# Kernel tuning notes

Hardware: AMD Instinct MI355X
Metric: run time of the kernel (lower is better)

The kernel has to match this reference:

```python
import jax, jax.numpy as jnp
import numpy as np

POOLED_H = 7
POOLED_W = 7
SPATIAL_SCALE = 0.0625
B, C, H, W = 8, 256, 48, 48
R = 300
IMG = 768  # = H / SPATIAL_SCALE


def setup_inputs() -> dict:
    key = jax.random.key(0)
    k1, k2, k3, k4 = jax.random.split(key, 4)
    features = jax.random.normal(k1, (B, C, H, W), dtype=jnp.float32)
    # rois: (batch_idx, x1, y1, x2, y2) in input-image coords
    bidx = jax.random.randint(k2, (R, 1), 0, B).astype(jnp.float32)
    tl = jax.random.uniform(k3, (R, 2), minval=0.0, maxval=IMG - 64.0)
    wh = jax.random.uniform(k4, (R, 2), minval=32.0, maxval=320.0)
    br = jnp.minimum(tl + wh, IMG - 1.0)
    rois = jnp.concatenate([bidx, tl, br], axis=1).astype(jnp.float32)
    return {"features": features, "rois": rois}


def _hat_integral(x, grid):
    """Integral from -inf to x of the unit hat basis function centered at each
    grid point g (support [g-1, g+1], peak 1, total mass 1).
    x: [..., 1-broadcastable], grid: [G] -> returns [..., G]."""
    t = x[..., None] - (grid - 1.0)
    return jnp.where(
        t <= 0.0, 0.0,
        jnp.where(t <= 1.0, 0.5 * t * t,
                  jnp.where(t <= 2.0, 1.0 - 0.5 * (2.0 - t) ** 2, 1.0)))


def reference(features, rois):
    # Precise RoI Pooling: exact double integral of the bilinear interpolant
    # over each bin, divided by bin area. Bilinear interp (with zero padding
    # outside the map, as in the CUDA PrRoIPoolingGetData) is
    #   f(u,v) = sum_{j,i} feat[j,i] * hat_j(v) * hat_i(u)
    # so the bin integral factorizes into per-axis hat-integral weights.
    Bf, Cf, Hf, Wf = features.shape
    bidx = rois[:, 0].astype(jnp.int32)
    x1 = rois[:, 1] * SPATIAL_SCALE
    y1 = rois[:, 2] * SPATIAL_SCALE
    x2 = rois[:, 3] * SPATIAL_SCALE
    y2 = rois[:, 4] * SPATIAL_SCALE
    roi_w = jnp.maximum(x2 - x1, 0.0)
    roi_h = jnp.maximum(y2 - y1, 0.0)
    bin_w = roi_w / POOLED_W  # [R]
    bin_h = roi_h / POOLED_H

    ph = jnp.arange(POOLED_H, dtype=jnp.float32)
    pw = jnp.arange(POOLED_W, dtype=jnp.float32)
    ya = y1[:, None] + ph[None, :] * bin_h[:, None]  # [R, PH]
    yb = ya + bin_h[:, None]
    xa = x1[:, None] + pw[None, :] * bin_w[:, None]  # [R, PW]
    xb = xa + bin_w[:, None]

    gy = jnp.arange(Hf, dtype=jnp.float32)
    gx = jnp.arange(Wf, dtype=jnp.float32)
    Wy = _hat_integral(yb, gy) - _hat_integral(ya, gy)  # [R, PH, H]
    Wx = _hat_integral(xb, gx) - _hat_integral(xa, gx)  # [R, PW, W]

    feat = features[bidx]  # [R, C, H, W]
    t = jnp.einsum('rpj,rcji->rcpi', Wy, feat)   # integrate over y
    num = jnp.einsum('rqi,rcpi->rcpq', Wx, t)    # integrate over x -> [R,C,PH,PW]

    area = (bin_w * bin_h)[:, None, None, None]  # win_size per ROI
    out = jnp.where(area > 0.0, num / jnp.where(area > 0.0, area, 1.0), 0.0)
    return out
```

## Files before the change

kernel.cpp:

```cpp
#include <hip/hip_runtime.h>


#define PH 7
#define PW 7
#define NBINS 49
#define SCALE 0.0625f
#define CH 256
#define FH 48
#define FW 48
#define RNUM 300
#define MAXJ 23
#define PRM 112
#define PATCHF (MAXJ * 28 * 2)
#define RSF 328

__device__ __forceinline__ float hat_int(float x, float g) {
    float t = x - (g - 1.0f);
    if (t <= 0.0f) return 0.0f;
    if (t <= 1.0f) return 0.5f * t * t;
    if (t <= 2.0f) { float u = 2.0f - t; return 1.0f - 0.5f * u * u; }
    return 1.0f;
}

__global__ __launch_bounds__(256)
void prroi_prep(const float* __restrict__ rois, float* __restrict__ prm) {
    const int r = blockIdx.x * 4 + (threadIdx.x >> 6);
    const int t = threadIdx.x & 63;
    if (r >= RNUM || t >= 15) return;

    const float* roi = rois + r * 5;
    const int   b  = (int)roi[0];
    const float x1 = roi[1] * SCALE, y1 = roi[2] * SCALE;
    const float x2 = roi[3] * SCALE, y2 = roi[4] * SCALE;
    const float roi_w = fmaxf(x2 - x1, 0.0f), roi_h = fmaxf(y2 - y1, 0.0f);
    const float bin_w = roi_w / (float)PW, bin_h = roi_h / (float)PH;
    const float area = bin_w * bin_h;
    const float inv_area = (area > 0.0f) ? (1.0f / area) : 0.0f;

    const float ylo = fminf(y1, y2), yhi = fmaxf(y1, y2);
    const float xlo = fminf(x1, x2), xhi = fmaxf(x1, x2);
    const int j1 = min(FH - 1, (int)floorf(yhi) + 1);
    const int i1 = min(FW - 1, (int)floorf(xhi) + 1);
    const int J0 = min(max(0, (int)floorf(ylo) - 1), FH - 6);
    const int I0 = min(max(0, (int)floorf(xlo) - 1) & ~3, FW - 8);
    const int JROWS = min(FH - J0, max(j1 - J0 + 1, 6));
    int NI4 = min(((i1 - I0) >> 2) + 1, (FW - I0) >> 2);
    NI4 = max(NI4, 2);

    float* p = prm + (size_t)r * PRM;
    if (t < PH) {
        const int ph = t;
        const float ya = y1 + ph * bin_h, yb = ya + bin_h;
        const int base = min(max((int)floorf(ya) - 1, J0), J0 + JROWS - 6);
        p[84 + ph] = __int_as_float(base - J0);
#pragma unroll
        for (int k = 0; k < 6; ++k) {
            const float g = (float)(base + k);
            p[ph * 6 + k] = hat_int(yb, g) - hat_int(ya, g);
        }
    } else if (t < PH + PW) {
        const int pw = t - PH;
        const float xa = x1 + pw * bin_w, xb = xa + bin_w;
        const int base = min(max((int)floorf(xa) - 1, I0), I0 + 4 * NI4 - 6);
        p[91 + pw] = __int_as_float(base - I0);
#pragma unroll
        for (int k = 0; k < 6; ++k) {
            const float g = (float)(base + k);
            p[42 + pw * 6 + k] = hat_int(xb, g) - hat_int(xa, g);
        }
    } else {
        p[98]  = inv_area;
        p[99]  = __int_as_float(b);
        p[100] = __int_as_float(J0);
        p[101] = __int_as_float(I0);
        p[102] = __int_as_float(JROWS);
        p[103] = __int_as_float(NI4);
    }
}

__global__ __launch_bounds__(256, 6)
void prroi_main(const float* __restrict__ feat,
                const float* __restrict__ prm,
                float* __restrict__ out) {
    const int wv   = threadIdx.x >> 6;
    const int lane = threadIdx.x & 63;
    const int r    = blockIdx.y;
    const int cblk = blockIdx.x * 4 + wv;
    const int c0   = cblk * 2;

    __shared__ float lds[4][PATCHF + RSF];
    float* patch = lds[wv];
    float* rsw   = lds[wv] + PATCHF;

    const float* p = prm + (size_t)r * PRM;
    const int b     = __float_as_int(p[99]);
    const int J0    = __float_as_int(p[100]);
    const int I0    = __float_as_int(p[101]);
    const int JROWS = __float_as_int(p[102]);
    const int NI4   = __float_as_int(p[103]);
    const float ia  = p[98];

    const int pwA = lane >> 3;
    const int jsl = lane & 7;
    const bool actA = lane < 56;
    float wx[6]; int bi = 0;
    if (actA) {
        bi = __float_as_int(p[91 + pwA]);
#pragma unroll
        for (int k = 0; k < 6; ++k) wx[k] = p[42 + pwA * 6 + k];
    }
    const bool actB = lane < NBINS;
    int bj = 0, pwB = 0;
    float wy[6];
    if (actB) {
        const int ph = lane / 7;
        pwB = lane - ph * 7;
        bj = __float_as_int(p[84 + ph]);
#pragma unroll
        for (int k = 0; k < 6; ++k) wy[k] = p[ph * 6 + k];
    }

    const float* fb = feat + (size_t)(b * CH + c0) * (FH * FW);
    const int NU = JROWS << 3;
    for (int u = lane; u < NU; u += 64) {
        const int j = u >> 3, i4 = u & 7;
        if (i4 < NI4) {
            const float* src = fb + (size_t)(J0 + j) * FW + I0 + 4 * i4;
            const float4 a = *(const float4*)src;
            const float4 c = *(const float4*)(src + FH * FW);
            const int base = j * 56 + 8 * i4;
            const int sw = (j & 7) << 1;
            *(float2*)&patch[(base + 0) ^ sw] = make_float2(a.x, c.x);
            *(float2*)&patch[(base + 2) ^ sw] = make_float2(a.y, c.y);
            *(float2*)&patch[(base + 4) ^ sw] = make_float2(a.z, c.z);
            *(float2*)&patch[(base + 6) ^ sw] = make_float2(a.w, c.w);
        }
    }
    asm volatile("s_waitcnt lgkmcnt(0)" ::: "memory");

    if (actA) {
        for (int j = jsl; j < JROWS; j += 8) {
            const int rowb = j * 56 + 2 * bi;
            const int sw = (j & 7) << 1;
            float ax = 0.0f, ay = 0.0f;
#pragma unroll
            for (int ii = 0; ii < 6; ++ii) {
                const float2 v = *(const float2*)&patch[(rowb + 2 * ii) ^ sw];
                ax += wx[ii] * v.x; ay += wx[ii] * v.y;
            }
            *(float2*)&rsw[(pwA * MAXJ + j) * 2] = make_float2(ax, ay);
        }
    }
    asm volatile("s_waitcnt lgkmcnt(0)" ::: "memory");

    if (actB) {
        float ax = 0.0f, ay = 0.0f;
#pragma unroll
        for (int jj = 0; jj < 6; ++jj) {
            const float2 v = *(const float2*)&rsw[(pwB * MAXJ + (bj + jj)) * 2];
            ax += wy[jj] * v.x; ay += wy[jj] * v.y;
        }
        float* o = out + ((size_t)r * CH + c0) * NBINS + lane;
        o[0]     = ax * ia;
        o[NBINS] = ay * ia;
    }
}

extern "C" void kernel_launch(void* const* d_in, const int* in_sizes, int n_in,
                              void* d_out, int out_size, void* d_ws, size_t ws_size,
                              hipStream_t stream) {
    const float* feat = (const float*)d_in[0];
    const float* rois = (const float*)d_in[1];
    float* out = (float*)d_out;
    float* prm = (float*)d_ws;

    prroi_prep<<<(RNUM + 3) / 4, 256, 0, stream>>>(rois, prm);
    prroi_main<<<dim3(32, RNUM), 256, 0, stream>>>(feat, prm, out);
}
```

Measured before the change: 86.36 us.

## Group ROIs by batch and reuse full feature map in LDS across ROIs

The prep kernel gains an extra block that builds per-batch ROI lists and counts. The main kernel now launches one block per (batch, channel pair), loads the whole 48x48 map for two channels into LDS once, and loops over every ROI of that batch. Before, each ROI block fetched its own patch, so the same feature data was read repeatedly from global memory. In exchange, ROI counts per batch are uneven, which causes load imbalance, and the grid shrinks to 1024 blocks of 128 threads, each using a large LDS allocation that limits occupancy.

```diff
diff --git a/kernel.cpp b/kernel.cpp
--- a/kernel.cpp
+++ b/kernel.cpp
@@ -9,10 +9,10 @@
 #define FH 48
 #define FW 48
 #define RNUM 300
-#define MAXJ 23
 #define PRM 112
-#define PATCHF (MAXJ * 28 * 2)
-#define RSF 328
+#define PRMF (RNUM * PRM)
+#define LISTCAP 304
+#define RSF 332
 
 __device__ __forceinline__ float hat_int(float x, float g) {
     float t = x - (g - 1.0f);
@@ -24,6 +24,27 @@
 
 __global__ __launch_bounds__(256)
 void prroi_prep(const float* __restrict__ rois, float* __restrict__ prm) {
+    if (blockIdx.x == 75) {
+        __shared__ int lb[RNUM];
+        int* lst = (int*)(prm + PRMF);
+        int* cnt = lst + 8 * LISTCAP;
+        const int tid = threadIdx.x;
+        for (int u = tid; u < RNUM; u += 256) lb[u] = (int)rois[5 * u];
+        __syncthreads();
+        for (int u = tid; u < RNUM; u += 256) {
+            const int bu = lb[u];
+            int pos = 0;
+            for (int r2 = 0; r2 < u; ++r2) pos += (lb[r2] == bu) ? 1 : 0;
+            lst[bu * LISTCAP + pos] = u;
+        }
+        if (tid < 8) {
+            int c = 0;
+            for (int r2 = 0; r2 < RNUM; ++r2) c += (lb[r2] == tid) ? 1 : 0;
+            cnt[tid] = c;
+        }
+        return;
+    }
+
     const int r = blockIdx.x * 4 + (threadIdx.x >> 6);
     const int t = threadIdx.x & 63;
     if (r >= RNUM || t >= 15) return;
@@ -78,91 +99,93 @@
     }
 }
 
-__global__ __launch_bounds__(256, 6)
+__global__ __launch_bounds__(128, 2)
 void prroi_main(const float* __restrict__ feat,
                 const float* __restrict__ prm,
                 float* __restrict__ out) {
-    const int wv   = threadIdx.x >> 6;
-    const int lane = threadIdx.x & 63;
-    const int r    = blockIdx.y;
-    const int cblk = blockIdx.x * 4 + wv;
-    const int c0   = cblk * 2;
-
-    __shared__ float lds[4][PATCHF + RSF];
-    float* patch = lds[wv];
-    float* rsw   = lds[wv] + PATCHF;
-
-    const float* p = prm + (size_t)r * PRM;
-    const int b     = __float_as_int(p[99]);
-    const int J0    = __float_as_int(p[100]);
-    const int I0    = __float_as_int(p[101]);
-    const int JROWS = __float_as_int(p[102]);
-    const int NI4   = __float_as_int(p[103]);
-    const float ia  = p[98];
-
-    const int pwA = lane >> 3;
-    const int jsl = lane & 7;
+    const int bid = blockIdx.x;
+    const int b   = bid >> 7;
+    const int c2  = bid & 127;
+    const int c0  = c2 * 2;
+    const int tid = threadIdx.x;
+    const int wv  = tid >> 6, lane = tid & 63;
+
+    __shared__ float patch[FH * FW * 2];
+    __shared__ float rsw[2][RSF];
+
+    const float* fb = feat + (size_t)(b * CH + c0) * (FH * FW);
+    for (int u = tid; u < (FH * FW / 4); u += 128) {
+        const int j  = u / 12;
+        const float4 a = *(const float4*)(fb + u * 4);
+        const float4 c = *(const float4*)(fb + FH * FW + u * 4);
+        const int o0 = u * 8;
+        const int sw = (j & 7) << 2;
+        *(float2*)&patch[(o0 + 0) ^ sw] = make_float2(a.x, c.x);
+        *(float2*)&patch[(o0 + 2) ^ sw] = make_float2(a.y, c.y);
+        *(float2*)&patch[(o0 + 4) ^ sw] = make_float2(a.z, c.z);
+        *(float2*)&patch[(o0 + 6) ^ sw] = make_float2(a.w, c.w);
+    }
+    __syncthreads();
+
+    const int* lst = (const int*)(prm + PRMF);
+    const int cnt  = lst[8 * LISTCAP + b];
+    float* rsme = rsw[wv];
+
+    const int  pwA  = lane >> 3, jsl = lane & 7;
     const bool actA = lane < 56;
-    float wx[6]; int bi = 0;
-    if (actA) {
-        bi = __float_as_int(p[91 + pwA]);
-#pragma unroll
-        for (int k = 0; k < 6; ++k) wx[k] = p[42 + pwA * 6 + k];
-    }
     const bool actB = lane < NBINS;
-    int bj = 0, pwB = 0;
-    float wy[6];
-    if (actB) {
-        const int ph = lane / 7;
-        pwB = lane - ph * 7;
-        bj = __float_as_int(p[84 + ph]);
-#pragma unroll
-        for (int k = 0; k < 6; ++k) wy[k] = p[ph * 6 + k];
-    }
-
-    const float* fb = feat + (size_t)(b * CH + c0) * (FH * FW);
-    const int NU = JROWS << 3;
-    for (int u = lane; u < NU; u += 64) {
-        const int j = u >> 3, i4 = u & 7;
-        if (i4 < NI4) {
-            const float* src = fb + (size_t)(J0 + j) * FW + I0 + 4 * i4;
-            const float4 a = *(const float4*)src;
-            const float4 c = *(const float4*)(src + FH * FW);
-            const int base = j * 56 + 8 * i4;
-            const int sw = (j & 7) << 1;
-            *(float2*)&patch[(base + 0) ^ sw] = make_float2(a.x, c.x);
-            *(float2*)&patch[(base + 2) ^ sw] = make_float2(a.y, c.y);
-            *(float2*)&patch[(base + 4) ^ sw] = make_float2(a.z, c.z);
-            *(float2*)&patch[(base + 6) ^ sw] = make_float2(a.w, c.w);
-        }
-    }
-    asm volatile("s_waitcnt lgkmcnt(0)" ::: "memory");
-
-    if (actA) {
-        for (int j = jsl; j < JROWS; j += 8) {
-            const int rowb = j * 56 + 2 * bi;
-            const int sw = (j & 7) << 1;
+    int phB = 0, pwB = 0;
+    if (actB) { phB = lane / 7; pwB = lane - phB * 7; }
+
+    for (int k = wv; k < cnt; k += 2) {
+        const int r = lst[b * LISTCAP + k];
+        const float* p = prm + (size_t)r * PRM;
+        const float ia = p[98];
+        const int J0    = __float_as_int(p[100]);
+        const int I0    = __float_as_int(p[101]);
+        const int JROWS = __float_as_int(p[102]);
+
+        float wx[6]; int biA = 0;
+        if (actA) {
+            biA = I0 + __float_as_int(p[91 + pwA]);
+#pragma unroll
+            for (int t6 = 0; t6 < 6; ++t6) wx[t6] = p[42 + pwA * 6 + t6];
+        }
+        float wy[6]; int bj = 0;
+        if (actB) {
+            bj = __float_as_int(p[84 + phB]);
+#pragma unroll
+            for (int t6 = 0; t6 < 6; ++t6) wy[t6] = p[phB * 6 + t6];
+        }
+
+        if (actA) {
+            for (int jr = jsl; jr < JROWS; jr += 8) {
+                const int j  = J0 + jr;
+                const int o0 = (j * FW + biA) * 2;
+                const int sw = (j & 7) << 2;
+                float ax = 0.0f, ay = 0.0f;
+#pragma unroll
+                for (int ii = 0; ii < 6; ++ii) {
+                    const float2 v = *(const float2*)&patch[(o0 + 2 * ii) ^ sw];
+                    ax += wx[ii] * v.x; ay += wx[ii] * v.y;
+                }
+                *(float2*)&rsme[(pwA * 23 + jr) * 2] = make_float2(ax, ay);
+            }
+        }
+        asm volatile("s_waitcnt lgkmcnt(0)" ::: "memory");
+
+        if (actB) {
             float ax = 0.0f, ay = 0.0f;
 #pragma unroll
-            for (int ii = 0; ii < 6; ++ii) {
-                const float2 v = *(const float2*)&patch[(rowb + 2 * ii) ^ sw];
-                ax += wx[ii] * v.x; ay += wx[ii] * v.y;
+            for (int jj = 0; jj < 6; ++jj) {
+                const float2 v = *(const float2*)&rsme[(pwB * 23 + bj + jj) * 2];
+                ax += wy[jj] * v.x; ay += wy[jj] * v.y;
             }
-            *(float2*)&rsw[(pwA * MAXJ + j) * 2] = make_float2(ax, ay);
-        }
-    }
-    asm volatile("s_waitcnt lgkmcnt(0)" ::: "memory");
-
-    if (actB) {
-        float ax = 0.0f, ay = 0.0f;
-#pragma unroll
-        for (int jj = 0; jj < 6; ++jj) {
-            const float2 v = *(const float2*)&rsw[(pwB * MAXJ + (bj + jj)) * 2];
-            ax += wy[jj] * v.x; ay += wy[jj] * v.y;
-        }
-        float* o = out + ((size_t)r * CH + c0) * NBINS + lane;
-        o[0]     = ax * ia;
-        o[NBINS] = ay * ia;
+            float* o = out + ((size_t)r * CH + c0) * NBINS + lane;
+            o[0]     = ax * ia;
+            o[NBINS] = ay * ia;
+        }
+        asm volatile("s_waitcnt lgkmcnt(0)" ::: "memory");
     }
 }
 
@@ -174,6 +197,6 @@
     float* out = (float*)d_out;
     float* prm = (float*)d_ws;
 
-    prroi_prep<<<(RNUM + 3) / 4, 256, 0, stream>>>(rois, prm);
-    prroi_main<<<dim3(32, RNUM), 256, 0, stream>>>(feat, prm, out);
-}
+    prroi_prep<<<76, 256, 0, stream>>>(rois, prm);
+    prroi_main<<<1024, 128, 0, stream>>>(feat, prm, out);
+}
```

Measured after the change: 110.5 us. 27.9% more time.

## Process four channels per wave with register-prefetched second channel pair

Applied to the files above, without the earlier changes.

Each wavefront now handles four channels instead of two, halving the grid. All patch loads for the second channel pair are issued up front into registers and written to LDS after the first pair is reduced, overlapping global latency with compute. The per-ROI parameter layout is padded to 8-float strides so weights and headers load as float4. The LDS XOR swizzle is removed, which may reintroduce bank conflicts, and register pressure increases.

```diff
diff --git a/kernel.cpp b/kernel.cpp
--- a/kernel.cpp
+++ b/kernel.cpp
@@ -9,9 +9,8 @@
 #define FH 48
 #define FW 48
 #define RNUM 300
-#define MAXJ 23
-#define PRM 112
-#define PATCHF (MAXJ * 28 * 2)
+#define PRM 128
+#define PATCHF (23 * 56)
 #define RSF 328
 
 __device__ __forceinline__ float hat_int(float x, float g) {
@@ -52,29 +51,29 @@
         const int ph = t;
         const float ya = y1 + ph * bin_h, yb = ya + bin_h;
         const int base = min(max((int)floorf(ya) - 1, J0), J0 + JROWS - 6);
-        p[84 + ph] = __int_as_float(base - J0);
+        p[ph * 8 + 6] = __int_as_float(base - J0);
 #pragma unroll
         for (int k = 0; k < 6; ++k) {
             const float g = (float)(base + k);
-            p[ph * 6 + k] = hat_int(yb, g) - hat_int(ya, g);
+            p[ph * 8 + k] = hat_int(yb, g) - hat_int(ya, g);
         }
     } else if (t < PH + PW) {
         const int pw = t - PH;
         const float xa = x1 + pw * bin_w, xb = xa + bin_w;
         const int base = min(max((int)floorf(xa) - 1, I0), I0 + 4 * NI4 - 6);
-        p[91 + pw] = __int_as_float(base - I0);
+        p[56 + pw * 8 + 6] = __int_as_float(base - I0);
 #pragma unroll
         for (int k = 0; k < 6; ++k) {
             const float g = (float)(base + k);
-            p[42 + pw * 6 + k] = hat_int(xb, g) - hat_int(xa, g);
+            p[56 + pw * 8 + k] = hat_int(xb, g) - hat_int(xa, g);
         }
     } else {
-        p[98]  = inv_area;
-        p[99]  = __int_as_float(b);
-        p[100] = __int_as_float(J0);
-        p[101] = __int_as_float(I0);
-        p[102] = __int_as_float(JROWS);
-        p[103] = __int_as_float(NI4);
+        p[112] = inv_area;
+        p[113] = __int_as_float(b);
+        p[114] = __int_as_float(J0);
+        p[115] = __int_as_float(I0);
+        p[116] = __int_as_float(JROWS);
+        p[117] = __int_as_float(NI4);
     }
 }
 
@@ -85,84 +84,136 @@
     const int wv   = threadIdx.x >> 6;
     const int lane = threadIdx.x & 63;
     const int r    = blockIdx.y;
-    const int cblk = blockIdx.x * 4 + wv;
-    const int c0   = cblk * 2;
+    const int c4   = blockIdx.x * 4 + wv;
+    const int c0   = c4 * 4;
 
     __shared__ float lds[4][PATCHF + RSF];
     float* patch = lds[wv];
     float* rsw   = lds[wv] + PATCHF;
 
     const float* p = prm + (size_t)r * PRM;
-    const int b     = __float_as_int(p[99]);
-    const int J0    = __float_as_int(p[100]);
-    const int I0    = __float_as_int(p[101]);
-    const int JROWS = __float_as_int(p[102]);
-    const int NI4   = __float_as_int(p[103]);
-    const float ia  = p[98];
-
-    const int pwA = lane >> 3;
-    const int jsl = lane & 7;
+    const float4 h0 = *(const float4*)(p + 112);
+    const float2 h1 = *(const float2*)(p + 116);
+    const float ia  = h0.x;
+    const int b     = __float_as_int(h0.y);
+    const int J0    = __float_as_int(h0.z);
+    const int I0    = __float_as_int(h0.w);
+    const int JROWS = __float_as_int(h1.x);
+    const int NI4   = __float_as_int(h1.y);
+
+    const int  pwA = lane >> 3, jsl = lane & 7;
     const bool actA = lane < 56;
-    float wx[6]; int bi = 0;
+    float wx0 = 0, wx1 = 0, wx2 = 0, wx3 = 0, wx4 = 0, wx5 = 0;
+    int biA = 0;
     if (actA) {
-        bi = __float_as_int(p[91 + pwA]);
-#pragma unroll
-        for (int k = 0; k < 6; ++k) wx[k] = p[42 + pwA * 6 + k];
+        const float4 wa = *(const float4*)(p + 56 + pwA * 8);
+        const float4 wb = *(const float4*)(p + 56 + pwA * 8 + 4);
+        wx0 = wa.x; wx1 = wa.y; wx2 = wa.z; wx3 = wa.w;
+        wx4 = wb.x; wx5 = wb.y; biA = __float_as_int(wb.z);
     }
     const bool actB = lane < NBINS;
-    int bj = 0, pwB = 0;
-    float wy[6];
+    float wy0 = 0, wy1 = 0, wy2 = 0, wy3 = 0, wy4 = 0, wy5 = 0;
+    int pwB = 0, bjB = 0;
     if (actB) {
         const int ph = lane / 7;
         pwB = lane - ph * 7;
-        bj = __float_as_int(p[84 + ph]);
-#pragma unroll
-        for (int k = 0; k < 6; ++k) wy[k] = p[ph * 6 + k];
-    }
-
+        const float4 ua = *(const float4*)(p + ph * 8);
+        const float4 ub = *(const float4*)(p + ph * 8 + 4);
+        wy0 = ua.x; wy1 = ua.y; wy2 = ua.z; wy3 = ua.w;
+        wy4 = ub.x; wy5 = ub.y; bjB = __float_as_int(ub.z);
+    }
+
+    const int NU = JROWS << 3;
     const float* fb = feat + (size_t)(b * CH + c0) * (FH * FW);
-    const int NU = JROWS << 3;
-    for (int u = lane; u < NU; u += 64) {
-        const int j = u >> 3, i4 = u & 7;
-        if (i4 < NI4) {
-            const float* src = fb + (size_t)(J0 + j) * FW + I0 + 4 * i4;
-            const float4 a = *(const float4*)src;
-            const float4 c = *(const float4*)(src + FH * FW);
-            const int base = j * 56 + 8 * i4;
-            const int sw = (j & 7) << 1;
-            *(float2*)&patch[(base + 0) ^ sw] = make_float2(a.x, c.x);
-            *(float2*)&patch[(base + 2) ^ sw] = make_float2(a.y, c.y);
-            *(float2*)&patch[(base + 4) ^ sw] = make_float2(a.z, c.z);
-            *(float2*)&patch[(base + 6) ^ sw] = make_float2(a.w, c.w);
+    const float* srcp[3];
+    bool act_[3]; int dst_[3];
+    float4 pa0[3], pa1[3], pb0[3], pb1[3];
+#pragma unroll
+    for (int s = 0; s < 3; ++s) {
+        const int u  = lane + (s << 6);
+        const int j  = u >> 3, i4 = u & 7;
+        const bool a = (u < NU) && (i4 < NI4);
+        act_[s] = a;
+        dst_[s] = j * 56 + 8 * i4;
+        srcp[s] = fb + (size_t)(J0 + j) * FW + I0 + 4 * i4;
+        if (a) {
+            pa0[s] = *(const float4*)(srcp[s]);
+            pa1[s] = *(const float4*)(srcp[s] + FH * FW);
+        }
+    }
+#pragma unroll
+    for (int s = 0; s < 3; ++s) {
+        if (act_[s]) {
+            pb0[s] = *(const float4*)(srcp[s] + 2 * FH * FW);
+            pb1[s] = *(const float4*)(srcp[s] + 3 * FH * FW);
+        }
+    }
+
+#pragma unroll
+    for (int s = 0; s < 3; ++s) {
+        if (act_[s]) {
+            float* d = patch + dst_[s];
+            *(float4*)(d + 0) = make_float4(pa0[s].x, pa1[s].x, pa0[s].y, pa1[s].y);
+            *(float4*)(d + 4) = make_float4(pa0[s].z, pa1[s].z, pa0[s].w, pa1[s].w);
         }
     }
     asm volatile("s_waitcnt lgkmcnt(0)" ::: "memory");
 
-    if (actA) {
-        for (int j = jsl; j < JROWS; j += 8) {
-            const int rowb = j * 56 + 2 * bi;
-            const int sw = (j & 7) << 1;
+#pragma unroll 1
+    for (int it = 0; it < 2; ++it) {
+        if (actA) {
+            for (int jr = jsl; jr < JROWS; jr += 8) {
+                const float* row = patch + jr * 56 + 2 * biA;
+                const float2 v0 = *(const float2*)(row + 0);
+                const float2 v1 = *(const float2*)(row + 2);
+                const float2 v2 = *(const float2*)(row + 4);
+                const float2 v3 = *(const float2*)(row + 6);
+                const float2 v4 = *(const float2*)(row + 8);
+                const float2 v5 = *(const float2*)(row + 10);
+                float ax = 0.0f, ay = 0.0f;
+                ax += wx0 * v0.x; ay += wx0 * v0.y;
+                ax += wx1 * v1.x; ay += wx1 * v1.y;
+                ax += wx2 * v2.x; ay += wx2 * v2.y;
+                ax += wx3 * v3.x; ay += wx3 * v3.y;
+                ax += wx4 * v4.x; ay += wx4 * v4.y;
+                ax += wx5 * v5.x; ay += wx5 * v5.y;
+                *(float2*)&rsw[(pwA * 23 + jr) * 2] = make_float2(ax, ay);
+            }
+        }
+        asm volatile("s_waitcnt lgkmcnt(0)" ::: "memory");
+
+        if (actB) {
+            const float* rb = rsw + (pwB * 23 + bjB) * 2;
+            const float2 u0 = *(const float2*)(rb + 0);
+            const float2 u1 = *(const float2*)(rb + 2);
+            const float2 u2 = *(const float2*)(rb + 4);
+            const float2 u3 = *(const float2*)(rb + 6);
+            const float2 u4 = *(const float2*)(rb + 8);
+            const float2 u5 = *(const float2*)(rb + 10);
             float ax = 0.0f, ay = 0.0f;
-#pragma unroll
-            for (int ii = 0; ii < 6; ++ii) {
-                const float2 v = *(const float2*)&patch[(rowb + 2 * ii) ^ sw];
-                ax += wx[ii] * v.x; ay += wx[ii] * v.y;
+            ax += wy0 * u0.x; ay += wy0 * u0.y;
+            ax += wy1 * u1.x; ay += wy1 * u1.y;
+            ax += wy2 * u2.x; ay += wy2 * u2.y;
+            ax += wy3 * u3.x; ay += wy3 * u3.y;
+            ax += wy4 * u4.x; ay += wy4 * u4.y;
+            ax += wy5 * u5.x; ay += wy5 * u5.y;
+            float* o = out + ((size_t)r * CH + c0 + 2 * it) * NBINS + lane;
+            o[0]     = ax * ia;
+            o[NBINS] = ay * ia;
+        }
+
+        if (it == 0) {
+            asm volatile("s_waitcnt lgkmcnt(0)" ::: "memory");
+#pragma unroll
+            for (int s = 0; s < 3; ++s) {
+                if (act_[s]) {
+                    float* d = patch + dst_[s];
+                    *(float4*)(d + 0) = make_float4(pb0[s].x, pb1[s].x, pb0[s].y, pb1[s].y);
+                    *(float4*)(d + 4) = make_float4(pb0[s].z, pb1[s].z, pb0[s].w, pb1[s].w);
+                }
             }
-            *(float2*)&rsw[(pwA * MAXJ + j) * 2] = make_float2(ax, ay);
-        }
-    }
-    asm volatile("s_waitcnt lgkmcnt(0)" ::: "memory");
-
-    if (actB) {
-        float ax = 0.0f, ay = 0.0f;
-#pragma unroll
-        for (int jj = 0; jj < 6; ++jj) {
-            const float2 v = *(const float2*)&rsw[(pwB * MAXJ + (bj + jj)) * 2];
-            ax += wy[jj] * v.x; ay += wy[jj] * v.y;
-        }
-        float* o = out + ((size_t)r * CH + c0) * NBINS + lane;
-        o[0]     = ax * ia;
-        o[NBINS] = ay * ia;
+            asm volatile("s_waitcnt lgkmcnt(0)" ::: "memory");
+        }
     }
 }
 
@@ -175,5 +226,5 @@
     float* prm = (float*)d_ws;
 
     prroi_prep<<<(RNUM + 3) / 4, 256, 0, stream>>>(rois, prm);
-    prroi_main<<<dim3(32, RNUM), 256, 0, stream>>>(feat, prm, out);
-}
+    prroi_main<<<dim3(16, RNUM), 256, 0, stream>>>(feat, prm, out);
+}
```

Measured after the change: 87.15 us. No clear change (+0.9%).
